# Optimization experiments

Hardware: AMD Instinct MI355X
Metric: run time of the kernel (lower is better)

Reference implementation:

```python
import jax, jax.numpy as jnp
import numpy as np

N_WAY = 64
EPS = 1e-5  # torch LayerNorm default


def _layernorm(x, g, b):
    mu = jnp.mean(x, axis=-1, keepdims=True)
    var = jnp.mean(jnp.square(x - mu), axis=-1, keepdims=True)
    return (x - mu) * jax.lax.rsqrt(var + EPS) * g + b


def _backbone(x, params):
    (W1, b1, g1, be1, W2, b2, g2, be2, W3, b3, g3, be3, W4, b4) = params
    h = jax.nn.relu(_layernorm(x @ W1.T + b1, g1, be1))
    h = jax.nn.relu(_layernorm(h @ W2.T + b2, g2, be2))
    h = jax.nn.relu(_layernorm(h @ W3.T + b3, g3, be3))
    return h @ W4.T + b4


def setup_inputs() -> dict:
    key = jax.random.key(0)
    ks = jax.random.split(key, 20)
    d = {}
    d["support_features"] = jax.random.normal(ks[0], (32768, 768), jnp.float32)
    d["support_labels"] = jax.random.randint(ks[1], (32768,), 0, N_WAY, jnp.int64)
    d["query_features"] = jax.random.normal(ks[2], (65536, 768), jnp.float32)
    dims = [(512, 768), (512, 512), (128, 512), (32, 128)]
    ki = 3
    for i, (dout, din) in enumerate(dims, start=1):
        scale = 1.0 / np.sqrt(din)
        d[f"W{i}"] = jax.random.uniform(ks[ki], (dout, din), jnp.float32, -scale, scale); ki += 1
        d[f"b{i}"] = jax.random.uniform(ks[ki], (dout,), jnp.float32, -scale, scale); ki += 1
        if i < 4:
            d[f"g{i}"] = jnp.ones((dout,), jnp.float32)
            d[f"be{i}"] = jnp.zeros((dout,), jnp.float32)
    return d


def reference(support_features, support_labels, query_features,
              W1, b1, g1, be1, W2, b2, g2, be2, W3, b3, g3, be3, W4, b4):
    params = (W1, b1, g1, be1, W2, b2, g2, be2, W3, b3, g3, be3, W4, b4)
    z_support = _backbone(support_features, params)   # [Ns, 32]
    z_query = _backbone(query_features, params)       # [Nq, 32]
    # segment-mean prototypes (replaces per-class nonzero+mean loop)
    sums = jax.ops.segment_sum(z_support, support_labels, num_segments=N_WAY)
    counts = jax.ops.segment_sum(jnp.ones((z_support.shape[0],), z_support.dtype),
                                 support_labels, num_segments=N_WAY)
    z_proto = sums / jnp.maximum(counts, 1.0)[:, None]  # [n_way, 32]
    # -cdist (euclidean)
    sq = (jnp.sum(z_query * z_query, axis=1)[:, None]
          + jnp.sum(z_proto * z_proto, axis=1)[None, :]
          - 2.0 * z_query @ z_proto.T)
    return -jnp.sqrt(jnp.maximum(sq, 0.0))  # [Nq, n_way]
```

## Files before the change

kernel.cpp:

```cpp
#include <hip/hip_runtime.h>

typedef unsigned short u16;
typedef short bf16x8 __attribute__((ext_vector_type(8)));
typedef float f32x16 __attribute__((ext_vector_type(16)));
typedef unsigned short u16x4v __attribute__((ext_vector_type(4)));
typedef unsigned short u16x8v __attribute__((ext_vector_type(8)));

#define LN_EPS 1e-5f

__device__ __forceinline__ u16 f2bf(float v) {
    unsigned x = __float_as_uint(v);
    x += 0x7fffu + ((x >> 16) & 1u);
    return (u16)(x >> 16);
}
__device__ __forceinline__ float bf2f(u16 u) {
    return __uint_as_float(((unsigned)u) << 16);
}

#define GLD16(gp, lp) __builtin_amdgcn_global_load_lds( \
    (const __attribute__((address_space(1))) void*)(gp), \
    (__attribute__((address_space(3))) void*)(lp), 16, 0, 0)

__global__ __launch_bounds__(256)
void swizzle_split(const float* __restrict__ src, u16* __restrict__ hi,
                   u16* __restrict__ lo, int R, int DIN)
{
    __shared__ __align__(16) u16 SH[2][24][17][8];
    const int tid  = threadIdx.x;
    const int row0 = blockIdx.x * 16;
    const int QK   = DIN / 16;
    const int kq0  = QK * blockIdx.y;
    const int NKC  = DIN / 32;

    const int slots = 16 * QK;
    for (int s = tid; s < slots; s += 256) {
        int row = s / QK, kq = s % QK;
        float4 v = *(const float4*)(src + (long)(row0 + row) * DIN + (long)(kq0 + kq) * 4);
        int kc = kq >> 1, jh = (kq & 1) * 4;
        float vv[4] = {v.x, v.y, v.z, v.w};
        u16x4v h, l;
#pragma unroll
        for (int j = 0; j < 4; ++j) {
            u16 hb = f2bf(vv[j]);
            h[j] = hb;
            l[j] = f2bf(vv[j] - bf2f(hb));
        }
        *(u16x4v*)(&SH[0][kc][row][jh]) = h;
        *(u16x4v*)(&SH[1][kc][row][jh]) = l;
    }
    __syncthreads();
    const int chunks = NKC * 16;
    for (int s = tid; s < chunks; s += 256) {
        int row = s & 15, kc = s >> 4;
        long o = ((long)(kq0 / 2 + kc) * R + row0 + row) * 8;
        *(u16x8v*)(hi + o) = *(const u16x8v*)(&SH[0][kc][row][0]);
        *(u16x8v*)(lo + o) = *(const u16x8v*)(&SH[1][kc][row][0]);
    }
}

template<int DOUT, int OUT_MODE, int NT, int TROWS>
__device__ __forceinline__ void ln_epilogue(
    f32x16 (&acc)[TROWS][NT], float (&lnp)[4][TROWS * 32][2],
    const float* __restrict__ bias, const float* __restrict__ gam,
    const float* __restrict__ bet,
    u16* __restrict__ Yh, u16* __restrict__ Yl, float* __restrict__ Yf,
    float* __restrict__ Hlds,
    long row0, int NR, int wv, int l31, int hh)
{
    float gg[NT], bb[NT], bev[NT];
#pragma unroll
    for (int u = 0; u < NT; ++u) {
        int c = wv * (DOUT / 4) + u * 32 + l31;
        bb[u] = bias[c]; gg[u] = gam[c]; bev[u] = bet[c];
    }
#pragma unroll
    for (int t = 0; t < TROWS; ++t)
#pragma unroll
        for (int r = 0; r < 16; ++r) {
            float s1 = 0.f, s2 = 0.f;
#pragma unroll
            for (int u = 0; u < NT; ++u) {
                float v = acc[t][u][r] + bb[u];
                acc[t][u][r] = v;
                s1 += v; s2 += v * v;
            }
#pragma unroll
            for (int off = 1; off < 32; off <<= 1) {
                s1 += __shfl_xor(s1, off, 64);
                s2 += __shfl_xor(s2, off, 64);
            }
            int row = t * 32 + (r & 3) + 8 * (r >> 2) + 4 * hh;
            if (l31 == r) { lnp[wv][row][0] = s1; lnp[wv][row][1] = s2; }
        }
    __syncthreads();
#pragma unroll
    for (int t = 0; t < TROWS; ++t)
#pragma unroll
        for (int r = 0; r < 16; ++r) {
            int row = t * 32 + (r & 3) + 8 * (r >> 2) + 4 * hh;
            float s1 = lnp[0][row][0] + lnp[1][row][0] + lnp[2][row][0] + lnp[3][row][0];
            float s2 = lnp[0][row][1] + lnp[1][row][1] + lnp[2][row][1] + lnp[3][row][1];
            float mean = s1 * (1.f / DOUT);
            float inv  = rsqrtf(s2 * (1.f / DOUT) - mean * mean + LN_EPS);
            long gr = row0 + row;
#pragma unroll
            for (int u = 0; u < NT; ++u) {
                int c = wv * (DOUT / 4) + u * 32 + l31;
                float v = (acc[t][u][r] - mean) * inv * gg[u] + bev[u];
                v = fmaxf(v, 0.f);
                if constexpr (OUT_MODE == 1) {
                    u16 hv = f2bf(v);
                    long o = ((long)(c >> 3) * NR + gr) * 8 + (c & 7);
                    Yh[o] = hv;
                    Yl[o] = f2bf(v - bf2f(hv));
                } else if constexpr (OUT_MODE == 2) {
                    Hlds[row * 129 + c] = v;
                } else {
                    Yf[gr * DOUT + c] = v;
                }
            }
        }
}

template<int NT, int TROWS>
__device__ __forceinline__ void mfma_step(
    const u16*& wph, const u16*& wpl, long wstep,
    const u16* AL0, const u16* AL1,
    f32x16 (&acc)[TROWS][NT], int l31)
{
    bf16x8 wf[NT][2], af[TROWS][2];
#pragma unroll
    for (int u = 0; u < NT; ++u) {
        wf[u][0] = *(const bf16x8*)(wph + u * 256);
        wf[u][1] = *(const bf16x8*)(wpl + u * 256);
    }
    wph += wstep; wpl += wstep;
#pragma unroll
    for (int t = 0; t < TROWS; ++t) {
        af[t][0] = *(const bf16x8*)(AL0 + (t * 32 + l31) * 8);
        af[t][1] = *(const bf16x8*)(AL1 + (t * 32 + l31) * 8);
    }
#pragma unroll
    for (int t = 0; t < TROWS; ++t)
#pragma unroll
        for (int u = 0; u < NT; ++u)
            acc[t][u] = __builtin_amdgcn_mfma_f32_32x32x16_bf16(af[t][0], wf[u][0], acc[t][u], 0, 0, 0);
#pragma unroll
    for (int t = 0; t < TROWS; ++t)
#pragma unroll
        for (int u = 0; u < NT; ++u)
            acc[t][u] = __builtin_amdgcn_mfma_f32_32x32x16_bf16(af[t][0], wf[u][1], acc[t][u], 0, 0, 0);
#pragma unroll
    for (int t = 0; t < TROWS; ++t)
#pragma unroll
        for (int u = 0; u < NT; ++u)
            acc[t][u] = __builtin_amdgcn_mfma_f32_32x32x16_bf16(af[t][1], wf[u][0], acc[t][u], 0, 0, 0);
}

template<int DOUT>
__global__ __launch_bounds__(256, 3)
void mfma_layer1_r32(const float* __restrict__ X,
                     const u16* __restrict__ Wh, const u16* __restrict__ Wl,
                     const float* __restrict__ bias, const float* __restrict__ gam,
                     const float* __restrict__ bet,
                     u16* __restrict__ Yh, u16* __restrict__ Yl,
                     int DIN, int NR, long rbase)
{
    constexpr int NT = DOUT / 128;
    __shared__ __align__(16) u16 AL[2][4][2][2][264];
    __shared__ float lnp[4][32][2];

    const int tid  = threadIdx.x;
    const int lane = tid & 63, wv = tid >> 6;
    const int l31  = lane & 31, hh = lane >> 5;
    const long lrow0 = (long)blockIdx.x * 32;
    const long row0  = rbase + lrow0;

    const int srow  = tid >> 3;
    const int kpart = tid & 7;
    const float* xp = X + (lrow0 + srow) * DIN + kpart * 8;

    const u16* wph = Wh + ((long)hh * DOUT + wv * (DOUT / 4) + l31) * 8;
    const u16* wpl = Wl + ((long)hh * DOUT + wv * (DOUT / 4) + l31) * 8;
    const long wstep = (long)2 * DOUT * 8;

    f32x16 acc[1][NT];
#pragma unroll
    for (int u = 0; u < NT; ++u)
#pragma unroll
        for (int e = 0; e < 16; ++e) acc[0][u][e] = 0.f;

    const int nslab = DIN / 64;

    auto stage = [&](const float* p, int buf) {
        float4 v0 = *(const float4*)(p);
        float4 v1 = *(const float4*)(p + 4);
        float f[8] = {v0.x, v0.y, v0.z, v0.w, v1.x, v1.y, v1.z, v1.w};
        u16x8v h, l;
#pragma unroll
        for (int j = 0; j < 8; ++j) {
            u16 hb = f2bf(f[j]);
            h[j] = hb;
            l[j] = f2bf(f[j] - bf2f(hb));
        }
        *(u16x8v*)(&AL[buf][kpart >> 1][0][kpart & 1][srow * 8]) = h;
        *(u16x8v*)(&AL[buf][kpart >> 1][1][kpart & 1][srow * 8]) = l;
    };

    stage(xp, 0);
    for (int sl = 0; sl < nslab; ++sl) {
        __syncthreads();
        const int cb = sl & 1;
        if (sl + 1 < nslab) stage(xp + (sl + 1) * 64, cb ^ 1);
#pragma unroll
        for (int s = 0; s < 4; ++s) {
            mfma_step<NT, 1>(wph, wpl, wstep,
                             &AL[cb][s][0][hh][0], &AL[cb][s][1][hh][0],
                             acc, l31);
        }
    }

    ln_epilogue<DOUT, 1, NT, 1>(acc, lnp, bias, gam, bet, Yh, Yl, nullptr,
                                nullptr, row0, NR, wv, l31, hh);
}

template<int DOUT>
__global__ __launch_bounds__(256, 3)
void mfma_layer_r32(const u16* __restrict__ Ah, const u16* __restrict__ Al,
                    const u16* __restrict__ Wh, const u16* __restrict__ Wl,
                    const float* __restrict__ bias, const float* __restrict__ gam,
                    const float* __restrict__ bet,
                    u16* __restrict__ Yh, u16* __restrict__ Yl,
                    int DIN, int NR)
{
    constexpr int NT = DOUT / 128;
    __shared__ __align__(16) u16 AL[2][4][2][2][256];
    __shared__ float lnp[4][32][2];

    const int tid  = threadIdx.x;
    const int lane = tid & 63, wv = tid >> 6;
    const int l31  = lane & 31, hh = lane >> 5;
    const long row0 = (long)blockIdx.x * 32;

    const u16* gp[2];
#pragma unroll
    for (int i = 0; i < 2; ++i) {
        const u16* base = i ? Al : Ah;
        gp[i] = base + ((long)(2 * wv + hh) * NR + row0 + l31) * 8;
    }
    const long stA = (long)8 * NR * 8;

    const u16* wph = Wh + ((long)hh * DOUT + wv * (DOUT / 4) + l31) * 8;
    const u16* wpl = Wl + ((long)hh * DOUT + wv * (DOUT / 4) + l31) * 8;
    const long wstep = (long)2 * DOUT * 8;

    f32x16 acc[1][NT];
#pragma unroll
    for (int u = 0; u < NT; ++u)
#pragma unroll
        for (int e = 0; e < 16; ++e) acc[0][u][e] = 0.f;

    const int nslab = DIN / 64;
#pragma unroll
    for (int i = 0; i < 2; ++i) {
        GLD16(gp[i], &AL[0][wv][i][0][0]);
        gp[i] += stA;
    }

    for (int sl = 0; sl < nslab; ++sl) {
        __syncthreads();
        const int cb = sl & 1;
        if (sl + 1 < nslab) {
#pragma unroll
            for (int i = 0; i < 2; ++i) {
                GLD16(gp[i], &AL[cb ^ 1][wv][i][0][0]);
                gp[i] += stA;
            }
        }
#pragma unroll
        for (int s = 0; s < 4; ++s) {
            mfma_step<NT, 1>(wph, wpl, wstep,
                             &AL[cb][s][0][hh][0], &AL[cb][s][1][hh][0],
                             acc, l31);
        }
    }

    ln_epilogue<DOUT, 1, NT, 1>(acc, lnp, bias, gam, bet, Yh, Yl, nullptr,
                                nullptr, row0, NR, wv, l31, hh);
}

template<int DOUT>
__global__ __launch_bounds__(256, 4)
void mfma_layer3(const u16* __restrict__ Ah, const u16* __restrict__ Al,
                 const u16* __restrict__ Wh, const u16* __restrict__ Wl,
                 const float* __restrict__ bias, const float* __restrict__ gam,
                 const float* __restrict__ bet,
                 float* __restrict__ Yf, int DIN, int NR,
                 const float* __restrict__ W4, const float* __restrict__ b4)
{
    constexpr int NT = DOUT / 128;
    __shared__ __align__(16) u16 AL[2][4][2][2][520];
    __shared__ float lnp[4][64][2];
    float* Hs = (float*)&AL[0][0][0][0][0];

    const int tid  = threadIdx.x;
    const int lane = tid & 63, wv = tid >> 6;
    const int l31  = lane & 31, hh = lane >> 5;
    const long row0 = (long)blockIdx.x * 64;

    const u16* gpA[4];
    const long stA = (long)8 * NR * 8;
#pragma unroll
    for (int t = 0; t < 4; ++t) {
        int p = t & 1, c = t >> 1;
        const u16* base = p ? Al : Ah;
        gpA[t] = base + ((long)(2 * wv + c) * NR + row0 + lane) * 8;
    }

    const u16* wph = Wh + ((long)hh * DOUT + wv * (DOUT / 4) + l31) * 8;
    const u16* wpl = Wl + ((long)hh * DOUT + wv * (DOUT / 4) + l31) * 8;
    const long wstep = (long)2 * DOUT * 8;

    f32x16 acc[2][NT];
#pragma unroll
    for (int t = 0; t < 2; ++t)
#pragma unroll
        for (int u = 0; u < NT; ++u)
#pragma unroll
            for (int e = 0; e < 16; ++e) acc[t][u][e] = 0.f;

    const int nslab = DIN / 64;
#pragma unroll
    for (int t = 0; t < 4; ++t) {
        GLD16(gpA[t], &AL[0][wv][t & 1][t >> 1][0]);
        gpA[t] += stA;
    }

    for (int sl = 0; sl < nslab; ++sl) {
        __syncthreads();
        const int cb = sl & 1;
        if (sl + 1 < nslab) {
#pragma unroll
            for (int t = 0; t < 4; ++t) {
                GLD16(gpA[t], &AL[cb ^ 1][wv][t & 1][t >> 1][0]);
                gpA[t] += stA;
            }
        }
#pragma unroll
        for (int s = 0; s < 4; ++s) {
            mfma_step<NT, 2>(wph, wpl, wstep,
                             &AL[cb][s][0][hh][0], &AL[cb][s][1][hh][0],
                             acc, l31);
        }
    }

    ln_epilogue<DOUT, 2, NT, 2>(acc, lnp, bias, gam, bet, nullptr, nullptr,
                                Yf, Hs, row0, NR, wv, l31, hh);

    __syncthreads();
    const int rowl = tid & 63;
    const int og   = wv;
    float a4[8];
#pragma unroll
    for (int j = 0; j < 8; ++j) a4[j] = 0.f;
    for (int k = 0; k < 128; k += 4) {
        float h0 = Hs[rowl * 129 + k + 0];
        float h1 = Hs[rowl * 129 + k + 1];
        float h2 = Hs[rowl * 129 + k + 2];
        float h3 = Hs[rowl * 129 + k + 3];
#pragma unroll
        for (int j = 0; j < 8; ++j) {
            const float4 w = *(const float4*)(W4 + (og * 8 + j) * 128 + k);
            a4[j] = fmaf(h0, w.x, fmaf(h1, w.y, fmaf(h2, w.z, fmaf(h3, w.w, a4[j]))));
        }
    }
    const long gr = row0 + rowl;
#pragma unroll
    for (int j = 0; j < 8; ++j) Yf[gr * 32 + og * 8 + j] = a4[j] + b4[og * 8 + j];
}

__global__ __launch_bounds__(256)
void proto_k(const float* __restrict__ Zs, const int* __restrict__ lab,
             float* __restrict__ P)
{
    const int c = blockIdx.x;
    const int tid = threadIdx.x, lane = tid & 63, wv = tid >> 6;
    float acc[32];
#pragma unroll
    for (int d = 0; d < 32; ++d) acc[d] = 0.f;
    float cnt = 0.f;
    for (int i = tid; i < 32768; i += 256) {
        if (lab[i] == c) {
            cnt += 1.f;
#pragma unroll
            for (int d = 0; d < 32; ++d) acc[d] += Zs[(long)i * 32 + d];
        }
    }
    __shared__ float wsum[4][32];
    __shared__ float wcnt[4];
#pragma unroll
    for (int d = 0; d < 32; ++d) {
        float v = acc[d];
        for (int off = 32; off > 0; off >>= 1) v += __shfl_xor(v, off, 64);
        if (lane == 0) wsum[wv][d] = v;
    }
    {
        float v = cnt;
        for (int off = 32; off > 0; off >>= 1) v += __shfl_xor(v, off, 64);
        if (lane == 0) wcnt[wv] = v;
    }
    __syncthreads();
    if (tid < 32) {
        float s  = wsum[0][tid] + wsum[1][tid] + wsum[2][tid] + wsum[3][tid];
        float cn = wcnt[0] + wcnt[1] + wcnt[2] + wcnt[3];
        P[c * 32 + tid] = s / fmaxf(cn, 1.f);
    }
}

__global__ __launch_bounds__(256)
void dist_k(const float* __restrict__ Zq, const float* __restrict__ P,
            float* __restrict__ O)
{
    __shared__ float ps[64 * 32];
    __shared__ float pn[64];
    const int tid = threadIdx.x;
    for (int idx = tid; idx < 2048; idx += 256) ps[idx] = P[idx];
    __syncthreads();
    if (tid < 64) {
        float s = 0.f;
        for (int d = 0; d < 32; ++d) { float v = ps[tid * 32 + d]; s += v * v; }
        pn[tid] = s;
    }
    __syncthreads();

    long q = (long)blockIdx.x * 256 + tid;
    float zr[32];
#pragma unroll
    for (int d = 0; d < 32; d += 4) {
        float4 v = *(const float4*)(Zq + q * 32 + d);
        zr[d] = v.x; zr[d + 1] = v.y; zr[d + 2] = v.z; zr[d + 3] = v.w;
    }
    float zz = 0.f;
#pragma unroll
    for (int d = 0; d < 32; ++d) zz += zr[d] * zr[d];
    for (int p = 0; p < 64; ++p) {
        float dot = 0.f;
#pragma unroll
        for (int d = 0; d < 32; ++d) dot = fmaf(zr[d], ps[p * 32 + d], dot);
        float sq = zz + pn[p] - 2.f * dot;
        O[q * 64 + p] = -sqrtf(fmaxf(sq, 0.f));
    }
}

extern "C" void kernel_launch(void* const* d_in, const int* in_sizes, int n_in,
                              void* d_out, int out_size, void* d_ws, size_t ws_size,
                              hipStream_t stream)
{
    const float* supp = (const float*)d_in[0];
    const int*   lab  = (const int*)  d_in[1];
    const float* qry  = (const float*)d_in[2];
    const float* W1 = (const float*)d_in[3];  const float* b1 = (const float*)d_in[4];
    const float* g1 = (const float*)d_in[5];  const float* be1= (const float*)d_in[6];
    const float* W2 = (const float*)d_in[7];  const float* b2 = (const float*)d_in[8];
    const float* g2 = (const float*)d_in[9];  const float* be2= (const float*)d_in[10];
    const float* W3 = (const float*)d_in[11]; const float* b3 = (const float*)d_in[12];
    const float* g3 = (const float*)d_in[13]; const float* be3= (const float*)d_in[14];
    const float* W4 = (const float*)d_in[15]; const float* b4 = (const float*)d_in[16];
    float* out = (float*)d_out;

    const long NTOT = 98304, NS = 32768, NQ = 65536;
    const int  NR = (int)NTOT;

    char* wsp = (char*)d_ws;
    size_t off = 0;
    auto take = [&](size_t bytes) {
        char* p = wsp + off;
        off += (bytes + 255) & ~(size_t)255;
        return (void*)p;
    };

    float* zAll  = (float*)take((size_t)NTOT * 32 * 4);
    float* proto = (float*)take(2048 * 4);
    u16* W1h = (u16*)take((size_t)512 * 768 * 2);
    u16* W1l = (u16*)take((size_t)512 * 768 * 2);
    u16* W2h = (u16*)take((size_t)512 * 512 * 2);
    u16* W2l = (u16*)take((size_t)512 * 512 * 2);
    u16* W3h = (u16*)take((size_t)128 * 512 * 2);
    u16* W3l = (u16*)take((size_t)128 * 512 * 2);
    u16* h1h = (u16*)take((size_t)NTOT * 512 * 2);
    u16* h1l = (u16*)take((size_t)NTOT * 512 * 2);
    u16* h2h = (u16*)take((size_t)NTOT * 512 * 2);
    u16* h2l = (u16*)take((size_t)NTOT * 512 * 2);

    swizzle_split<<<dim3(32, 4), dim3(256), 0, stream>>>(W1, W1h, W1l, 512, 768);
    swizzle_split<<<dim3(32, 4), dim3(256), 0, stream>>>(W2, W2h, W2l, 512, 512);
    swizzle_split<<<dim3(8, 4),  dim3(256), 0, stream>>>(W3, W3h, W3l, 128, 512);

    mfma_layer1_r32<512><<<dim3(NS / 32), dim3(256), 0, stream>>>(
        supp, W1h, W1l, b1, g1, be1, h1h, h1l, 768, NR, 0);
    mfma_layer1_r32<512><<<dim3(NQ / 32), dim3(256), 0, stream>>>(
        qry, W1h, W1l, b1, g1, be1, h1h, h1l, 768, NR, NS);

    mfma_layer_r32<512><<<dim3(NTOT / 32), dim3(256), 0, stream>>>(
        h1h, h1l, W2h, W2l, b2, g2, be2, h2h, h2l, 512, NR);
    mfma_layer3<128><<<dim3(NTOT / 64), dim3(256), 0, stream>>>(
        h2h, h2l, W3h, W3l, b3, g3, be3, zAll, 512, NR, W4, b4);

    proto_k<<<dim3(64),  dim3(256), 0, stream>>>(zAll, lab, proto);
    dist_k<<<dim3(256), dim3(256), 0, stream>>>(zAll + NS * 32, proto, out);
}
```

Baseline: 1.080 ms.

## Enlarge layer1/layer2 MFMA tiles to 128 rows with 8 waves per block

Layers 1 and 2 now use 512-thread blocks that each process 128 rows instead of 32, with 8 waves splitting the output columns and each wave holding 4 row tiles of accumulators. The aim is to reuse each weight fragment loaded from global memory across more rows, which cuts weight traffic per row. The LN epilogue is generalized to a variable number of waves. In exchange each thread holds more accumulator registers and the block uses more LDS, which lowers occupancy.

```diff
diff --git a/kernel.cpp b/kernel.cpp
--- a/kernel.cpp
+++ b/kernel.cpp
@@ -58,9 +58,9 @@
     }
 }
 
-template<int DOUT, int OUT_MODE, int NT, int TROWS>
+template<int DOUT, int OUT_MODE, int NT, int TROWS, int NW>
 __device__ __forceinline__ void ln_epilogue(
-    f32x16 (&acc)[TROWS][NT], float (&lnp)[4][TROWS * 32][2],
+    f32x16 (&acc)[TROWS][NT], float (&lnp)[NW][TROWS * 32][2],
     const float* __restrict__ bias, const float* __restrict__ gam,
     const float* __restrict__ bet,
     u16* __restrict__ Yh, u16* __restrict__ Yl, float* __restrict__ Yf,
@@ -70,7 +70,7 @@
     float gg[NT], bb[NT], bev[NT];
 #pragma unroll
     for (int u = 0; u < NT; ++u) {
-        int c = wv * (DOUT / 4) + u * 32 + l31;
+        int c = wv * (NT * 32) + u * 32 + l31;
         bb[u] = bias[c]; gg[u] = gam[c]; bev[u] = bet[c];
     }
 #pragma unroll
@@ -98,14 +98,15 @@
 #pragma unroll
         for (int r = 0; r < 16; ++r) {
             int row = t * 32 + (r & 3) + 8 * (r >> 2) + 4 * hh;
-            float s1 = lnp[0][row][0] + lnp[1][row][0] + lnp[2][row][0] + lnp[3][row][0];
-            float s2 = lnp[0][row][1] + lnp[1][row][1] + lnp[2][row][1] + lnp[3][row][1];
+            float s1 = 0.f, s2 = 0.f;
+#pragma unroll
+            for (int w = 0; w < NW; ++w) { s1 += lnp[w][row][0]; s2 += lnp[w][row][1]; }
             float mean = s1 * (1.f / DOUT);
             float inv  = rsqrtf(s2 * (1.f / DOUT) - mean * mean + LN_EPS);
             long gr = row0 + row;
 #pragma unroll
             for (int u = 0; u < NT; ++u) {
-                int c = wv * (DOUT / 4) + u * 32 + l31;
+                int c = wv * (NT * 32) + u * 32 + l31;
                 float v = (acc[t][u][r] - mean) * inv * gg[u] + bev[u];
                 v = fmaxf(v, 0.f);
                 if constexpr (OUT_MODE == 1) {
@@ -158,53 +159,59 @@
 }
 
 template<int DOUT>
-__global__ __launch_bounds__(256, 3)
-void mfma_layer1_r32(const float* __restrict__ X,
-                     const u16* __restrict__ Wh, const u16* __restrict__ Wl,
-                     const float* __restrict__ bias, const float* __restrict__ gam,
-                     const float* __restrict__ bet,
-                     u16* __restrict__ Yh, u16* __restrict__ Yl,
-                     int DIN, int NR, long rbase)
-{
-    constexpr int NT = DOUT / 128;
-    __shared__ __align__(16) u16 AL[2][4][2][2][264];
-    __shared__ float lnp[4][32][2];
+__global__ __launch_bounds__(512, 2)
+void mfma_layer1_b128(const float* __restrict__ X,
+                      const u16* __restrict__ Wh, const u16* __restrict__ Wl,
+                      const float* __restrict__ bias, const float* __restrict__ gam,
+                      const float* __restrict__ bet,
+                      u16* __restrict__ Yh, u16* __restrict__ Yl,
+                      int DIN, int NR, long rbase)
+{
+    constexpr int NT = DOUT / 256;
+    constexpr int TROWS = 4;
+    __shared__ __align__(16) u16 AL[2][4][2][2][1040];
+    __shared__ float lnp[8][128][2];
 
     const int tid  = threadIdx.x;
     const int lane = tid & 63, wv = tid >> 6;
     const int l31  = lane & 31, hh = lane >> 5;
-    const long lrow0 = (long)blockIdx.x * 32;
+    const long lrow0 = (long)blockIdx.x * 128;
     const long row0  = rbase + lrow0;
 
-    const int srow  = tid >> 3;
-    const int kpart = tid & 7;
-    const float* xp = X + (lrow0 + srow) * DIN + kpart * 8;
-
-    const u16* wph = Wh + ((long)hh * DOUT + wv * (DOUT / 4) + l31) * 8;
-    const u16* wpl = Wl + ((long)hh * DOUT + wv * (DOUT / 4) + l31) * 8;
+    const int srow  = tid >> 2;
+    const int kpart = tid & 3;
+    const float* xp = X + (lrow0 + srow) * DIN + kpart * 16;
+
+    const u16* wph = Wh + ((long)hh * DOUT + wv * (NT * 32) + l31) * 8;
+    const u16* wpl = Wl + ((long)hh * DOUT + wv * (NT * 32) + l31) * 8;
     const long wstep = (long)2 * DOUT * 8;
 
-    f32x16 acc[1][NT];
-#pragma unroll
-    for (int u = 0; u < NT; ++u)
-#pragma unroll
-        for (int e = 0; e < 16; ++e) acc[0][u][e] = 0.f;
+    f32x16 acc[TROWS][NT];
+#pragma unroll
+    for (int t = 0; t < TROWS; ++t)
+#pragma unroll
+        for (int u = 0; u < NT; ++u)
+#pragma unroll
+            for (int e = 0; e < 16; ++e) acc[t][u][e] = 0.f;
 
     const int nslab = DIN / 64;
 
     auto stage = [&](const float* p, int buf) {
-        float4 v0 = *(const float4*)(p);
-        float4 v1 = *(const float4*)(p + 4);
-        float f[8] = {v0.x, v0.y, v0.z, v0.w, v1.x, v1.y, v1.z, v1.w};
-        u16x8v h, l;
-#pragma unroll
-        for (int j = 0; j < 8; ++j) {
-            u16 hb = f2bf(f[j]);
-            h[j] = hb;
-            l[j] = f2bf(f[j] - bf2f(hb));
-        }
-        *(u16x8v*)(&AL[buf][kpart >> 1][0][kpart & 1][srow * 8]) = h;
-        *(u16x8v*)(&AL[buf][kpart >> 1][1][kpart & 1][srow * 8]) = l;
+#pragma unroll
+        for (int c = 0; c < 2; ++c) {
+            float4 v0 = *(const float4*)(p + c * 8);
+            float4 v1 = *(const float4*)(p + c * 8 + 4);
+            float f[8] = {v0.x, v0.y, v0.z, v0.w, v1.x, v1.y, v1.z, v1.w};
+            u16x8v h, l;
+#pragma unroll
+            for (int j = 0; j < 8; ++j) {
+                u16 hb = f2bf(f[j]);
+                h[j] = hb;
+                l[j] = f2bf(f[j] - bf2f(hb));
+            }
+            *(u16x8v*)(&AL[buf][kpart][0][c][srow * 8]) = h;
+            *(u16x8v*)(&AL[buf][kpart][1][c][srow * 8]) = l;
+        }
     };
 
     stage(xp, 0);
@@ -213,58 +220,63 @@
         const int cb = sl & 1;
         if (sl + 1 < nslab) stage(xp + (sl + 1) * 64, cb ^ 1);
 #pragma unroll
-        for (int s = 0; s < 4; ++s) {
-            mfma_step<NT, 1>(wph, wpl, wstep,
-                             &AL[cb][s][0][hh][0], &AL[cb][s][1][hh][0],
-                             acc, l31);
-        }
-    }
-
-    ln_epilogue<DOUT, 1, NT, 1>(acc, lnp, bias, gam, bet, Yh, Yl, nullptr,
-                                nullptr, row0, NR, wv, l31, hh);
+        for (int s = 0; s < 4; ++s)
+            mfma_step<NT, TROWS>(wph, wpl, wstep,
+                                 &AL[cb][s][0][hh][0], &AL[cb][s][1][hh][0],
+                                 acc, l31);
+    }
+
+    ln_epilogue<DOUT, 1, NT, TROWS, 8>(acc, lnp, bias, gam, bet, Yh, Yl,
+                                       nullptr, nullptr, row0, NR, wv, l31, hh);
 }
 
 template<int DOUT>
-__global__ __launch_bounds__(256, 3)
-void mfma_layer_r32(const u16* __restrict__ Ah, const u16* __restrict__ Al,
-                    const u16* __restrict__ Wh, const u16* __restrict__ Wl,
-                    const float* __restrict__ bias, const float* __restrict__ gam,
-                    const float* __restrict__ bet,
-                    u16* __restrict__ Yh, u16* __restrict__ Yl,
-                    int DIN, int NR)
-{
-    constexpr int NT = DOUT / 128;
-    __shared__ __align__(16) u16 AL[2][4][2][2][256];
-    __shared__ float lnp[4][32][2];
+__global__ __launch_bounds__(512, 2)
+void mfma_layer_b128(const u16* __restrict__ Ah, const u16* __restrict__ Al,
+                     const u16* __restrict__ Wh, const u16* __restrict__ Wl,
+                     const float* __restrict__ bias, const float* __restrict__ gam,
+                     const float* __restrict__ bet,
+                     u16* __restrict__ Yh, u16* __restrict__ Yl,
+                     int DIN, int NR)
+{
+    constexpr int NT = DOUT / 256;
+    constexpr int TROWS = 4;
+    __shared__ __align__(16) u16 AL[2][4][2][2][1024];
+    __shared__ float lnp[8][128][2];
 
     const int tid  = threadIdx.x;
     const int lane = tid & 63, wv = tid >> 6;
     const int l31  = lane & 31, hh = lane >> 5;
-    const long row0 = (long)blockIdx.x * 32;
-
-    const u16* gp[2];
-#pragma unroll
-    for (int i = 0; i < 2; ++i) {
-        const u16* base = i ? Al : Ah;
-        gp[i] = base + ((long)(2 * wv + hh) * NR + row0 + l31) * 8;
+    const long row0 = (long)blockIdx.x * 128;
+
+    const u16* gp[4];
+    int sj[4], pj[4], cj[4], hj[4];
+#pragma unroll
+    for (int j = 0; j < 4; ++j) {
+        int i = wv * 4 + j;
+        sj[j] = i >> 3; pj[j] = (i >> 2) & 1; cj[j] = (i >> 1) & 1; hj[j] = i & 1;
+        const u16* base = pj[j] ? Al : Ah;
+        gp[j] = base + ((long)(sj[j] * 2 + cj[j]) * NR + row0 + hj[j] * 64 + lane) * 8;
     }
     const long stA = (long)8 * NR * 8;
 
-    const u16* wph = Wh + ((long)hh * DOUT + wv * (DOUT / 4) + l31) * 8;
-    const u16* wpl = Wl + ((long)hh * DOUT + wv * (DOUT / 4) + l31) * 8;
+    const u16* wph = Wh + ((long)hh * DOUT + wv * (NT * 32) + l31) * 8;
+    const u16* wpl = Wl + ((long)hh * DOUT + wv * (NT * 32) + l31) * 8;
     const long wstep = (long)2 * DOUT * 8;
 
-    f32x16 acc[1][NT];
-#pragma unroll
-    for (int u = 0; u < NT; ++u)
-#pragma unroll
-        for (int e = 0; e < 16; ++e) acc[0][u][e] = 0.f;
+    f32x16 acc[TROWS][NT];
+#pragma unroll
+    for (int t = 0; t < TROWS; ++t)
+#pragma unroll
+        for (int u = 0; u < NT; ++u)
+#pragma unroll
+            for (int e = 0; e < 16; ++e) acc[t][u][e] = 0.f;
 
     const int nslab = DIN / 64;
 #pragma unroll
-    for (int i = 0; i < 2; ++i) {
-        GLD16(gp[i], &AL[0][wv][i][0][0]);
-        gp[i] += stA;
+    for (int j = 0; j < 4; ++j) {
+        GLD16(gp[j], &AL[0][sj[j]][pj[j]][cj[j]][hj[j] * 512]);
+        gp[j] += stA;
     }
 
     for (int sl = 0; sl < nslab; ++sl) {
@@ -272,21 +284,20 @@
         const int cb = sl & 1;
         if (sl + 1 < nslab) {
 #pragma unroll
-            for (int i = 0; i < 2; ++i) {
-                GLD16(gp[i], &AL[cb ^ 1][wv][i][0][0]);
-                gp[i] += stA;
+            for (int j = 0; j < 4; ++j) {
+                GLD16(gp[j], &AL[cb ^ 1][sj[j]][pj[j]][cj[j]][hj[j] * 512]);
+                gp[j] += stA;
             }
         }
 #pragma unroll
-        for (int s = 0; s < 4; ++s) {
-            mfma_step<NT, 1>(wph, wpl, wstep,
-                             &AL[cb][s][0][hh][0], &AL[cb][s][1][hh][0],
-                             acc, l31);
-        }
-    }
-
-    ln_epilogue<DOUT, 1, NT, 1>(acc, lnp, bias, gam, bet, Yh, Yl, nullptr,
-                                nullptr, row0, NR, wv, l31, hh);
+        for (int s = 0; s < 4; ++s)
+            mfma_step<NT, TROWS>(wph, wpl, wstep,
+                                 &AL[cb][s][0][hh][0], &AL[cb][s][1][hh][0],
+                                 acc, l31);
+    }
+
+    ln_epilogue<DOUT, 1, NT, TROWS, 8>(acc, lnp, bias, gam, bet, Yh, Yl,
+                                       nullptr, nullptr, row0, NR, wv, l31, hh);
 }
 
 template<int DOUT>
@@ -299,6 +310,7 @@
                  const float* __restrict__ W4, const float* __restrict__ b4)
 {
     constexpr int NT = DOUT / 128;
+    constexpr int TROWS = 2;
     __shared__ __align__(16) u16 AL[2][4][2][2][520];
     __shared__ float lnp[4][64][2];
     float* Hs = (float*)&AL[0][0][0][0][0];
@@ -321,9 +333,9 @@
     const u16* wpl = Wl + ((long)hh * DOUT + wv * (DOUT / 4) + l31) * 8;
     const long wstep = (long)2 * DOUT * 8;
 
-    f32x16 acc[2][NT];
-#pragma unroll
-    for (int t = 0; t < 2; ++t)
+    f32x16 acc[TROWS][NT];
+#pragma unroll
+    for (int t = 0; t < TROWS; ++t)
 #pragma unroll
         for (int u = 0; u < NT; ++u)
 #pragma unroll
@@ -347,15 +359,14 @@
             }
         }
 #pragma unroll
-        for (int s = 0; s < 4; ++s) {
-            mfma_step<NT, 2>(wph, wpl, wstep,
-                             &AL[cb][s][0][hh][0], &AL[cb][s][1][hh][0],
-                             acc, l31);
-        }
-    }
-
-    ln_epilogue<DOUT, 2, NT, 2>(acc, lnp, bias, gam, bet, nullptr, nullptr,
-                                Yf, Hs, row0, NR, wv, l31, hh);
+        for (int s = 0; s < 4; ++s)
+            mfma_step<NT, TROWS>(wph, wpl, wstep,
+                                 &AL[cb][s][0][hh][0], &AL[cb][s][1][hh][0],
+                                 acc, l31);
+    }
+
+    ln_epilogue<DOUT, 2, NT, TROWS, 4>(acc, lnp, bias, gam, bet, nullptr,
+                                       nullptr, Yf, Hs, row0, NR, wv, l31, hh);
 
     __syncthreads();
     const int rowl = tid & 63;
@@ -496,12 +507,12 @@
     swizzle_split<<<dim3(32, 4), dim3(256), 0, stream>>>(W2, W2h, W2l, 512, 512);
     swizzle_split<<<dim3(8, 4),  dim3(256), 0, stream>>>(W3, W3h, W3l, 128, 512);
 
-    mfma_layer1_r32<512><<<dim3(NS / 32), dim3(256), 0, stream>>>(
+    mfma_layer1_b128<512><<<dim3(NS / 128), dim3(512), 0, stream>>>(
         supp, W1h, W1l, b1, g1, be1, h1h, h1l, 768, NR, 0);
-    mfma_layer1_r32<512><<<dim3(NQ / 32), dim3(256), 0, stream>>>(
+    mfma_layer1_b128<512><<<dim3(NQ / 128), dim3(512), 0, stream>>>(
         qry, W1h, W1l, b1, g1, be1, h1h, h1l, 768, NR, NS);
 
-    mfma_layer_r32<512><<<dim3(NTOT / 32), dim3(256), 0, stream>>>(
+    mfma_layer_b128<512><<<dim3(NTOT / 128), dim3(512), 0, stream>>>(
         h1h, h1l, W2h, W2l, b2, g2, be2, h2h, h2l, 512, NR);
     mfma_layer3<128><<<dim3(NTOT / 64), dim3(256), 0, stream>>>(
         h2h, h2l, W3h, W3l, b3, g3, be3, zAll, 512, NR, W4, b4);
```

Result: no change. 1.091 ms (+1.1%).
